# Kernel optimization log

Hardware: AMD Instinct MI355X
Metric: run time of the kernel (lower is better)

The kernel has to match this reference:

```python
import jax, jax.numpy as jnp
import numpy as np

HEADS = 8

def setup_inputs() -> dict:
    key = jax.random.key(0)
    ks = jax.random.split(key, 7)
    B, T, D = 2, 4096, 512
    x = jax.random.normal(ks[0], (B, T, D), dtype=jnp.float32)
    s = 1.0 / np.sqrt(D)
    Wk = jax.random.uniform(ks[1], (D, D), jnp.float32, -s, s)
    bk = jax.random.uniform(ks[2], (D,), jnp.float32, -s, s)
    Wq = jax.random.uniform(ks[3], (D, D), jnp.float32, -s, s)
    bq = jax.random.uniform(ks[4], (D,), jnp.float32, -s, s)
    Wv = jax.random.uniform(ks[5], (D, D), jnp.float32, -s, s)
    bv = jax.random.uniform(ks[6], (D,), jnp.float32, -s, s)
    return {"x": x, "Wk": Wk, "bk": bk, "Wq": Wq, "bq": bq, "Wv": Wv, "bv": bv}

def reference(x, Wk, bk, Wq, bq, Wv, bv):
    B, T, D = x.shape
    H = HEADS
    hd = D // H
    # torch Linear: y = x @ W.T + b
    keys = (x @ Wk.T + bk).reshape(B, T, H, hd).transpose(0, 2, 1, 3)      # [B,H,T,hd]
    queries = (x @ Wq.T + bq).reshape(B, T, H, hd).transpose(0, 2, 1, 3)
    values = (x @ Wv.T + bv).reshape(B, T, H, hd).transpose(0, 2, 1, 3)
    scale = 1.0 / np.sqrt(hd)
    # NOTE: faithful to source — scores = K @ Q^T (not Q @ K^T)
    scores = jnp.einsum('bhkd,bhqd->bhkq', keys, queries) * scale          # [B,H,T,T]
    attn = jax.nn.softmax(scores, axis=-1)
    out = jnp.einsum('bhkq,bhqd->bhkd', attn, values)                      # [B,H,T,hd]
    return out.transpose(0, 2, 1, 3).reshape(B, T, D)
```

## Files before the change

### kernel.cpp

```cpp
#include <hip/hip_runtime.h>
#include <math.h>

#define TT 4096
#define DM 512
#define NH 8
#define HD 64
#define WN (DM * DM)

typedef float f32x4 __attribute__((ext_vector_type(4)));
typedef _Float16 half8 __attribute__((ext_vector_type(8)));

#define GLD16(gp, lp) __builtin_amdgcn_global_load_lds( \
    (const __attribute__((address_space(1))) void*)(gp), \
    (__attribute__((address_space(3))) void*)(lp), 16, 0, 0)

static __device__ __forceinline__ void splitf16(float x, unsigned short& hi, unsigned short& lo) {
    _Float16 h = (_Float16)x;
    hi = __builtin_bit_cast(unsigned short, h);
    _Float16 l = (_Float16)(x - (float)h);
    lo = __builtin_bit_cast(unsigned short, l);
}
static __device__ __forceinline__ int qperm(int r) {
    return ((r >> 5) << 5) | (((r >> 2) & 3) << 3) | (((r >> 4) & 1) << 2) | (r & 3);
}

__global__ __launch_bounds__(256) void wsplit(
    const float* __restrict__ Wq, const float* __restrict__ Wk, const float* __restrict__ Wv,
    unsigned short* __restrict__ Whi, unsigned short* __restrict__ Wlo)
{
    const int z = blockIdx.y;
    const float* __restrict__ src = (z == 0) ? Wq : (z == 1) ? Wk : Wv;
    const int i = (blockIdx.x * 256 + threadIdx.x) * 8;
    float4 a = *(const float4*)&src[i];
    float4 b = *(const float4*)&src[i + 4];
    float v[8] = {a.x, a.y, a.z, a.w, b.x, b.y, b.z, b.w};
    unsigned short hb[8], lb[8];
    #pragma unroll
    for (int k = 0; k < 8; ++k) splitf16(v[k], hb[k], lb[k]);
    uint4 hv, lv;
    hv.x = (unsigned int)hb[0] | ((unsigned int)hb[1] << 16);
    hv.y = (unsigned int)hb[2] | ((unsigned int)hb[3] << 16);
    hv.z = (unsigned int)hb[4] | ((unsigned int)hb[5] << 16);
    hv.w = (unsigned int)hb[6] | ((unsigned int)hb[7] << 16);
    lv.x = (unsigned int)lb[0] | ((unsigned int)lb[1] << 16);
    lv.y = (unsigned int)lb[2] | ((unsigned int)lb[3] << 16);
    lv.z = (unsigned int)lb[4] | ((unsigned int)lb[5] << 16);
    lv.w = (unsigned int)lb[6] | ((unsigned int)lb[7] << 16);
    *(uint4*)&Whi[(size_t)z * WN + i] = hv;
    *(uint4*)&Wlo[(size_t)z * WN + i] = lv;
}

__global__ __launch_bounds__(256, 3) void proj_mfma(
    const float* __restrict__ X,
    const unsigned short* __restrict__ Whi, const unsigned short* __restrict__ Wlo,
    const float* __restrict__ bq, const float* __restrict__ bk, const float* __restrict__ bv,
    unsigned short* __restrict__ Qh, unsigned short* __restrict__ Kh,
    unsigned short* __restrict__ Vt)
{
    const int z = blockIdx.z;
    const int m0 = blockIdx.x * 128;
    const int n0 = blockIdx.y * 128;
    const int tid = threadIdx.x;
    const int wid = tid >> 6, lane = tid & 63;
    const int lg = lane >> 4, lr = lane & 15;
    const int wr = (wid >> 1) * 64;
    const int wc = (wid & 1) * 64;

    __shared__ __attribute__((aligned(16))) unsigned short smem[128 * 72 + 2 * 128 * 64];
    auto Xs  = (unsigned short(*)[72])(smem);
    unsigned short* Ws0 = smem + 128 * 72;
    unsigned short* Ws1 = Ws0 + 128 * 64;

    const unsigned short* __restrict__ Wh = Whi + (size_t)z * WN;
    const unsigned short* __restrict__ Wl = Wlo + (size_t)z * WN;

    f32x4 acc[4][4];
    #pragma unroll
    for (int mt = 0; mt < 4; ++mt)
        #pragma unroll
        for (int nt = 0; nt < 4; ++nt) acc[mt][nt] = (f32x4){0.f, 0.f, 0.f, 0.f};

    const int xr = tid >> 1;
    const int xc = (tid & 1) * 32;

    for (int k0 = 0; k0 < DM; k0 += 64) {
        #pragma unroll
        for (int w = 0; w < 4; ++w) {
            float4 fa = *(const float4*)&X[(size_t)(m0 + xr) * DM + k0 + xc + w * 8];
            float4 fb = *(const float4*)&X[(size_t)(m0 + xr) * DM + k0 + xc + w * 8 + 4];
            float v[8] = {fa.x, fa.y, fa.z, fa.w, fb.x, fb.y, fb.z, fb.w};
            unsigned int hw[4];
            #pragma unroll
            for (int k = 0; k < 4; ++k) {
                unsigned short h0 = __builtin_bit_cast(unsigned short, (_Float16)v[2 * k]);
                unsigned short h1 = __builtin_bit_cast(unsigned short, (_Float16)v[2 * k + 1]);
                hw[k] = (unsigned int)h0 | ((unsigned int)h1 << 16);
            }
            uint4 hv = {hw[0], hw[1], hw[2], hw[3]};
            *(uint4*)&Xs[xr][xc + w * 8] = hv;
        }
        #pragma unroll
        for (int it = 0; it < 4; ++it) {
            int gi = it * 256 + tid;
            int fr = gi >> 3;
            int c  = (gi & 7) ^ (fr & 7);
            int dst = (it * 256 + wid * 64) * 16;
            GLD16(&Wh[(size_t)(n0 + fr) * DM + k0 + c * 8], (char*)Ws0 + dst);
            GLD16(&Wl[(size_t)(n0 + fr) * DM + k0 + c * 8], (char*)Ws1 + dst);
        }
        __syncthreads();

        __builtin_amdgcn_s_setprio(1);
        #pragma unroll
        for (int kc = 0; kc < 2; ++kc) {
            half8 xa[4];
            #pragma unroll
            for (int mt = 0; mt < 4; ++mt)
                xa[mt] = __builtin_bit_cast(half8, *(const int4*)&Xs[wr + mt * 16 + lr][kc * 32 + lg * 8]);
            #pragma unroll
            for (int nt = 0; nt < 4; ++nt) {
                int row = wc + nt * 16 + lr;
                int so = row * 128 + ((kc * 4 + lg) ^ (row & 7)) * 16;
                half8 wh = __builtin_bit_cast(half8, *(const int4*)((const char*)Ws0 + so));
                half8 wl = __builtin_bit_cast(half8, *(const int4*)((const char*)Ws1 + so));
                #pragma unroll
                for (int mt = 0; mt < 4; ++mt) {
                    acc[mt][nt] = __builtin_amdgcn_mfma_f32_16x16x32_f16(xa[mt], wh, acc[mt][nt], 0, 0, 0);
                    acc[mt][nt] = __builtin_amdgcn_mfma_f32_16x16x32_f16(xa[mt], wl, acc[mt][nt], 0, 0, 0);
                }
            }
        }
        __builtin_amdgcn_s_setprio(0);
        __syncthreads();
    }

    if (z < 2) {
        const float* __restrict__ bias = (z == 0) ? bq : bk;
        unsigned short* __restrict__ Dst = (z == 0) ? Qh : Kh;
        const float sc = (z == 0) ? 0.18033688f : 1.0f;
        #pragma unroll
        for (int nt = 0; nt < 4; ++nt) {
            int n = n0 + wc + nt * 16 + lr;
            float bv_ = bias[n];
            #pragma unroll
            for (int mt = 0; mt < 4; ++mt)
                #pragma unroll
                for (int r = 0; r < 4; ++r) {
                    int m = m0 + wr + mt * 16 + lg * 4 + r;
                    float y = (acc[mt][nt][r] + bv_) * sc;
                    Dst[(size_t)m * DM + n] =
                        __builtin_bit_cast(unsigned short, (_Float16)y);
                }
        }
    } else {
        unsigned short* Tk = (unsigned short*)smem;
        #pragma unroll
        for (int nt = 0; nt < 4; ++nt) {
            int d = wc + nt * 16 + lr;
            float bv_ = bv[n0 + d];
            #pragma unroll
            for (int mt = 0; mt < 4; ++mt)
                #pragma unroll
                for (int r = 0; r < 4; ++r) {
                    int t = wr + mt * 16 + lg * 4 + r;
                    float y = acc[mt][nt][r] + bv_;
                    Tk[d * 136 + t] = __builtin_bit_cast(unsigned short, (_Float16)y);
                }
        }
        __syncthreads();
        const int dl = tid >> 1, tq = tid & 1;
        const int bb = m0 >> 12, t0 = m0 & (TT - 1);
        const int hh = (n0 >> 6) + (dl >> 6);
        const int d = dl & 63;
        size_t obase = ((size_t)((bb * NH + hh) * HD + d)) * TT + t0 + tq * 64;
        #pragma unroll
        for (int j = 0; j < 8; ++j) {
            uint4 wv = *(const uint4*)&Tk[dl * 136 + tq * 64 + j * 8];
            *(uint4*)&Vt[obase + j * 8] = wv;
        }
    }
}

__global__ __launch_bounds__(256, 2) void attn_mfma(
    const unsigned short* __restrict__ Qh, const unsigned short* __restrict__ Kh,
    const unsigned short* __restrict__ Vt,
    float* __restrict__ Out)
{
    const int flat = blockIdx.x;
    const int bh = flat & 15;
    const int r0 = (flat >> 4) * 128;
    const int b = bh >> 3, h = bh & 7;
    const int tid = threadIdx.x;
    const int wid = tid >> 6, lane = tid & 63;
    const int lg = lane >> 4, lr = lane & 15;
    const int wr0 = r0 + wid * 32;

    __shared__ __attribute__((aligned(16))) unsigned short Qs[4][64][64];
    __shared__ __attribute__((aligned(16))) unsigned short Vs[4][64][64];

    const size_t qbase = (size_t)b * TT * DM + h * HD;
    const size_t vbase = ((size_t)(b * NH + h)) * HD * TT;

    half8 kf[2][2];
    #pragma unroll
    for (int rt = 0; rt < 2; ++rt)
        #pragma unroll
        for (int kc = 0; kc < 2; ++kc) {
            size_t g = qbase + (size_t)(wr0 + rt * 16 + lr) * DM + kc * 32 + lg * 8;
            kf[rt][kc] = __builtin_bit_cast(half8, *(const int4*)&Kh[g]);
        }

    half8 ones;
    {
        _Float16 o = (_Float16)((lr == 0) ? 1.0f : 0.0f);
        #pragma unroll
        for (int j = 0; j < 8; ++j) ones[j] = o;
    }

    const unsigned short* qp[2];
    const unsigned short* vp[2];
    int slds[2];
    #pragma unroll
    for (int it = 0; it < 2; ++it) {
        int gi = it * 256 + tid;
        int fr = gi >> 3;
        int ch = (gi & 7) ^ (fr & 7);
        qp[it] = Qh + qbase + (size_t)qperm(fr) * DM + ch * 8;
        vp[it] = Vt + vbase + (size_t)fr * TT + ch * 8;
        slds[it] = (it * 256 + wid * 64) * 16;
    }

    float m_s[2];
    f32x4 lacc[2];
    f32x4 oacc[2][4];
    #pragma unroll
    for (int rt = 0; rt < 2; ++rt) {
        m_s[rt] = -INFINITY;
        lacc[rt] = (f32x4){0.f, 0.f, 0.f, 0.f};
        #pragma unroll
        for (int dt = 0; dt < 4; ++dt) oacc[rt][dt] = (f32x4){0.f, 0.f, 0.f, 0.f};
    }

    auto QK = [&](int tau, f32x4 (&sacc)[2][4]) {
        #pragma unroll
        for (int rt = 0; rt < 2; ++rt)
            #pragma unroll
            for (int qt = 0; qt < 4; ++qt) sacc[rt][qt] = (f32x4){0.f, 0.f, 0.f, 0.f};
        __builtin_amdgcn_s_setprio(1);
        #pragma unroll
        for (int kc = 0; kc < 2; ++kc) {
            #pragma unroll
            for (int qt = 0; qt < 4; ++qt) {
                int row = qt * 16 + lr;
                int so = ((kc * 4 + lg) ^ (row & 7)) * 16;
                half8 qv = __builtin_bit_cast(half8, *(const int4*)((const char*)&Qs[tau][row][0] + so));
                #pragma unroll
                for (int rt = 0; rt < 2; ++rt)
                    sacc[rt][qt] = __builtin_amdgcn_mfma_f32_16x16x32_f16(qv, kf[rt][kc], sacc[rt][qt], 0, 0, 0);
            }
        }
        __builtin_amdgcn_s_setprio(0);
    };

    auto SMPV = [&](int tau, f32x4 (&sacc)[2][4]) {
        unsigned int hp[2][4][2];
        #pragma unroll
        for (int rt = 0; rt < 2; ++rt) {
            float mx = -INFINITY;
            #pragma unroll
            for (int qt = 0; qt < 4; ++qt)
                #pragma unroll
                for (int r = 0; r < 4; ++r) mx = fmaxf(mx, sacc[rt][qt][r]);
            if (!__all(mx - m_s[rt] <= 12.0f)) {
                mx = fmaxf(mx, __shfl_xor(mx, 16));
                mx = fmaxf(mx, __shfl_xor(mx, 32));
                float nm = fmaxf(m_s[rt], mx);
                float al = __builtin_amdgcn_exp2f(m_s[rt] - nm);
                m_s[rt] = nm;
                #pragma unroll
                for (int dt = 0; dt < 4; ++dt)
                    #pragma unroll
                    for (int r = 0; r < 4; ++r) oacc[rt][dt][r] *= al;
                #pragma unroll
                for (int r = 0; r < 4; ++r) lacc[rt][r] *= al;
            }
            const float nmb = m_s[rt];
            #pragma unroll
            for (int qt = 0; qt < 4; ++qt)
                #pragma unroll
                for (int r = 0; r < 4; ++r)
                    sacc[rt][qt][r] = __builtin_amdgcn_exp2f(sacc[rt][qt][r] - nmb);
            #pragma unroll
            for (int qt = 0; qt < 4; ++qt)
                #pragma unroll
                for (int pp = 0; pp < 2; ++pp)
                    hp[rt][qt][pp] = __builtin_bit_cast(unsigned int,
                        __builtin_amdgcn_cvt_pkrtz(sacc[rt][qt][2 * pp], sacc[rt][qt][2 * pp + 1]));
        }
        __builtin_amdgcn_s_setprio(1);
        #pragma unroll
        for (int c = 0; c < 2; ++c) {
            half8 pf[2];
            #pragma unroll
            for (int rt = 0; rt < 2; ++rt) {
                int4 ph4 = {(int)hp[rt][2 * c][0], (int)hp[rt][2 * c][1],
                            (int)hp[rt][2 * c + 1][0], (int)hp[rt][2 * c + 1][1]};
                pf[rt] = __builtin_bit_cast(half8, ph4);
            }
            #pragma unroll
            for (int rt = 0; rt < 2; ++rt)
                lacc[rt] = __builtin_amdgcn_mfma_f32_16x16x32_f16(ones, pf[rt], lacc[rt], 0, 0, 0);
            #pragma unroll
            for (int dt = 0; dt < 4; ++dt) {
                int row = dt * 16 + lr;
                int so = ((c * 4 + lg) ^ (row & 7)) * 16;
                half8 vh = __builtin_bit_cast(half8, *(const int4*)((const char*)&Vs[tau][row][0] + so));
                #pragma unroll
                for (int rt = 0; rt < 2; ++rt)
                    oacc[rt][dt] = __builtin_amdgcn_mfma_f32_16x16x32_f16(vh, pf[rt], oacc[rt][dt], 0, 0, 0);
            }
        }
        __builtin_amdgcn_s_setprio(0);
    };

    f32x4 sA[2][4], sB[2][4];

    for (int t = 0; t < TT / 256; ++t) {
        #pragma unroll
        for (int tau = 0; tau < 4; ++tau) {
            #pragma unroll
            for (int it = 0; it < 2; ++it) {
                GLD16(qp[it] + (size_t)tau * 64 * DM, (char*)&Qs[tau][0][0] + slds[it]);
                GLD16(vp[it] + tau * 64,              (char*)&Vs[tau][0][0] + slds[it]);
            }
        }
        #pragma unroll
        for (int it = 0; it < 2; ++it) { qp[it] += 256 * DM; vp[it] += 256; }
        __syncthreads();

        QK(0, sA);
        QK(1, sB); SMPV(0, sA);
        QK(2, sA); SMPV(1, sB);
        QK(3, sB); SMPV(2, sA);
                   SMPV(3, sB);
        __syncthreads();
    }

    #pragma unroll
    for (int rt = 0; rt < 2; ++rt) {
        float lfull = __shfl(lacc[rt][0], lr);
        float inv = __builtin_amdgcn_rcpf(lfull);
        int row = wr0 + rt * 16 + lr;
        #pragma unroll
        for (int dt = 0; dt < 4; ++dt)
            #pragma unroll
            for (int r = 0; r < 4; ++r)
                Out[((size_t)(b * TT + row)) * DM + h * HD + dt * 16 + lg * 4 + r] =
                    oacc[rt][dt][r] * inv;
    }
}

extern "C" void kernel_launch(void* const* d_in, const int* in_sizes, int n_in,
                              void* d_out, int out_size, void* d_ws, size_t ws_size,
                              hipStream_t stream)
{
    const float* x  = (const float*)d_in[0];
    const float* Wk = (const float*)d_in[1];
    const float* bk = (const float*)d_in[2];
    const float* Wq = (const float*)d_in[3];
    const float* bq = (const float*)d_in[4];
    const float* Wv = (const float*)d_in[5];
    const float* bv = (const float*)d_in[6];
    float* out = (float*)d_out;

    const size_t SZ = (size_t)2 * TT * DM;
    unsigned short* Qh  = (unsigned short*)d_ws;
    unsigned short* Kh  = Qh + SZ;
    unsigned short* Vt  = Kh + SZ;
    unsigned short* Whi = Vt + SZ;
    unsigned short* Wlo = Whi + (size_t)3 * WN;

    wsplit<<<dim3(WN / 2048, 3), dim3(256), 0, stream>>>(Wq, Wk, Wv, Whi, Wlo);

    dim3 pgrid(2 * TT / 128, DM / 128, 3);
    proj_mfma<<<pgrid, dim3(256), 0, stream>>>(x, Whi, Wlo, bq, bk, bv,
                                               Qh, Kh, Vt);

    attn_mfma<<<dim3(512), dim3(256), 0, stream>>>(Qh, Kh, Vt, out);
}
```

Before: 131.8 us.

## Double-buffer Q/V LDS tiles and prefetch the next 128-row chunk during compute

The main loop used to stage a full 256-query chunk of Q and V into shared memory, wait at a barrier, compute, and then wait at a second barrier, so loads and MFMA work never overlapped. It now splits LDS into two 128-query buffers. Each iteration issues async global-to-LDS loads for the next chunk while running QK and softmax/PV on the current one, leaving a single barrier per iteration. In exchange there are twice as many iterations and barriers, less QK/SMPV interleaving per iteration, and one redundant wrap-around prefetch on the final iteration.

```diff
diff --git a/kernel.cpp b/kernel.cpp
--- a/kernel.cpp
+++ b/kernel.cpp
@@ -195,8 +195,8 @@
     const int lg = lane >> 4, lr = lane & 15;
     const int wr0 = r0 + wid * 32;
 
-    __shared__ __attribute__((aligned(16))) unsigned short Qs[4][64][64];
-    __shared__ __attribute__((aligned(16))) unsigned short Vs[4][64][64];
+    __shared__ __attribute__((aligned(16))) unsigned short Qs[2][2][64][64];
+    __shared__ __attribute__((aligned(16))) unsigned short Vs[2][2][64][64];
 
     const size_t qbase = (size_t)b * TT * DM + h * HD;
     const size_t vbase = ((size_t)(b * NH + h)) * HD * TT;
@@ -230,6 +230,19 @@
         slds[it] = (it * 256 + wid * 64) * 16;
     }
 
+    auto STAGE = [&](int bufi, int q0) {
+        #pragma unroll
+        for (int tau = 0; tau < 2; ++tau) {
+            #pragma unroll
+            for (int it = 0; it < 2; ++it) {
+                GLD16(qp[it] + (size_t)(q0 + tau * 64) * DM,
+                      (char*)&Qs[bufi][tau][0][0] + slds[it]);
+                GLD16(vp[it] + q0 + tau * 64,
+                      (char*)&Vs[bufi][tau][0][0] + slds[it]);
+            }
+        }
+    };
+
     float m_s[2];
     f32x4 lacc[2];
     f32x4 oacc[2][4];
@@ -241,7 +254,7 @@
         for (int dt = 0; dt < 4; ++dt) oacc[rt][dt] = (f32x4){0.f, 0.f, 0.f, 0.f};
     }
 
-    auto QK = [&](int tau, f32x4 (&sacc)[2][4]) {
+    auto QK = [&](int cur, int tau, f32x4 (&sacc)[2][4]) {
         #pragma unroll
         for (int rt = 0; rt < 2; ++rt)
             #pragma unroll
@@ -253,7 +266,8 @@
             for (int qt = 0; qt < 4; ++qt) {
                 int row = qt * 16 + lr;
                 int so = ((kc * 4 + lg) ^ (row & 7)) * 16;
-                half8 qv = __builtin_bit_cast(half8, *(const int4*)((const char*)&Qs[tau][row][0] + so));
+                half8 qv = __builtin_bit_cast(half8,
+                    *(const int4*)((const char*)&Qs[cur][tau][row][0] + so));
                 #pragma unroll
                 for (int rt = 0; rt < 2; ++rt)
                     sacc[rt][qt] = __builtin_amdgcn_mfma_f32_16x16x32_f16(qv, kf[rt][kc], sacc[rt][qt], 0, 0, 0);
@@ -262,7 +276,7 @@
         __builtin_amdgcn_s_setprio(0);
     };
 
-    auto SMPV = [&](int tau, f32x4 (&sacc)[2][4]) {
+    auto SMPV = [&](int cur, int tau, f32x4 (&sacc)[2][4]) {
         unsigned int hp[2][4][2];
         #pragma unroll
         for (int rt = 0; rt < 2; ++rt) {
@@ -314,7 +328,8 @@
             for (int dt = 0; dt < 4; ++dt) {
                 int row = dt * 16 + lr;
                 int so = ((c * 4 + lg) ^ (row & 7)) * 16;
-                half8 vh = __builtin_bit_cast(half8, *(const int4*)((const char*)&Vs[tau][row][0] + so));
+                half8 vh = __builtin_bit_cast(half8,
+                    *(const int4*)((const char*)&Vs[cur][tau][row][0] + so));
                 #pragma unroll
                 for (int rt = 0; rt < 2; ++rt)
                     oacc[rt][dt] = __builtin_amdgcn_mfma_f32_16x16x32_f16(vh, pf[rt], oacc[rt][dt], 0, 0, 0);
@@ -325,24 +340,17 @@
 
     f32x4 sA[2][4], sB[2][4];
 
-    for (int t = 0; t < TT / 256; ++t) {
-        #pragma unroll
-        for (int tau = 0; tau < 4; ++tau) {
-            #pragma unroll
-            for (int it = 0; it < 2; ++it) {
-                GLD16(qp[it] + (size_t)tau * 64 * DM, (char*)&Qs[tau][0][0] + slds[it]);
-                GLD16(vp[it] + tau * 64,              (char*)&Vs[tau][0][0] + slds[it]);
-            }
-        }
-        #pragma unroll
-        for (int it = 0; it < 2; ++it) { qp[it] += 256 * DM; vp[it] += 256; }
-        __syncthreads();
-
-        QK(0, sA);
-        QK(1, sB); SMPV(0, sA);
-        QK(2, sA); SMPV(1, sB);
-        QK(3, sB); SMPV(2, sA);
-                   SMPV(3, sB);
+    STAGE(0, 0);
+    __syncthreads();
+
+    for (int t = 0; t < TT / 128; ++t) {
+        const int cur = t & 1;
+        STAGE(cur ^ 1, ((t + 1) * 128) & (TT - 1));
+
+        QK(cur, 0, sA);
+        QK(cur, 1, sB); SMPV(cur, 0, sA);
+                        SMPV(cur, 1, sB);
+
         __syncthreads();
     }
 
```

Result: no change. 129.6 us (-1.6%).
